# Kernel tuning notes

Hardware: AMD Instinct MI355X
Metric: run time of the kernel (lower is better)

Reference implementation:

```python
import jax, jax.numpy as jnp
import numpy as np

NSTEP = 5

# Clauses (vals = one-hot satisfying truth value per literal):
#   clause 0: ~S(x) | C(x)          vals: L0=[1,0], L1=[0,1]
#   clause 1: ~F(x,y) | ~S(x) | S(y) vals: L0=[1,0], L1=[1,0], L2=[0,1]
# Message to target literal i (torch influence()):
#   msg = w[r] * einsum over shared vars of prod_j ( q[pn_j] . (1 - vals_j) ) outer t_vals

def setup_inputs() -> dict:
    B, N = 2, 2048
    key = jax.random.key(0)
    k1, k2, k3 = jax.random.split(key, 3)
    return {
        "logits_S": jax.random.normal(k1, (B, N, 2), jnp.float32),
        "logits_C": jax.random.normal(k2, (B, N, 2), jnp.float32),
        "logits_F": jax.random.normal(k3, (B, N, N, 2), jnp.float32),
        "weights": jnp.ones((2,), jnp.float32),
    }


def _messages(qS, qC, qF, weights):
    dt = qS.dtype
    e_true = jnp.array([0.0, 1.0], dtype=dt)   # one-hot: positive literal satisfied
    e_false = jnp.array([1.0, 0.0], dtype=dt)  # one-hot: negated literal satisfied
    w0, w1 = weights[0], weights[1]
    # clause 0: ~S(x) | C(x)
    msg_C = (w0 * qS[..., 1])[..., None] * e_true            # [B,N,2]
    msg_S = (w0 * qC[..., 0])[..., None] * e_false           # [B,N,2]
    # clause 1: ~F(x,y) | ~S(x) | S(y)
    # target F(x,y): (q_S[b,x,true]) * (q_S[b,y,false]) on the 'false' slot of F
    msg_F = (w1 * qS[:, :, None, 1] * qS[:, None, :, 0])[..., None] * e_false  # [B,N,N,2]
    # target ~S(x): sum_y q_F[b,x,y,true] * q_S[b,y,false]
    msg_S = msg_S + (w1 * jnp.einsum('bxy,by->bx', qF[..., 1], qS[..., 0]))[..., None] * e_false
    # target S(y): sum_x q_F[b,x,y,true] * q_S[b,x,true]
    msg_S = msg_S + (w1 * jnp.einsum('bxy,bx->by', qF[..., 1], qS[..., 1]))[..., None] * e_true
    return msg_S, msg_C, msg_F


def reference(logits_S, logits_C, logits_F, weights):
    cur_S, cur_C, cur_F = logits_S, logits_C, logits_F
    for _ in range(NSTEP):
        qS = jax.nn.softmax(cur_S, axis=-1)
        qC = jax.nn.softmax(cur_C, axis=-1)
        qF = jax.nn.softmax(cur_F, axis=-1)
        msg_S, msg_C, msg_F = _messages(qS, qC, qF, weights)
        cur_S = logits_S + msg_S
        cur_C = logits_C + msg_C
        cur_F = logits_F + msg_F
    return (cur_S, cur_C, cur_F)
```

## Files before the change

kernel.cpp:

```cpp
#include <hip/hip_runtime.h>

#define NN   2048
#define ROWS 4096
#define RPB  16
#define CSPLIT 4
#define NBY  (ROWS/RPB)
#define PSTR 257
#define NBLK (CSPLIT*NBY)

#define SUBW 32
#define NSUB (NBLK/SUBW)
#define CPAD 16
#define BARSTRIDE ((NSUB+1)*CPAD)
#define NBAR 5
#define SPIN_LIMIT (1<<21)

__device__ __forceinline__ float fsig(float x) {
    float e = __expf(-x);
    return __builtin_amdgcn_rcpf(1.0f + e);
}

__device__ __forceinline__ float gload(const float* p) {
    return __hip_atomic_load(p, __ATOMIC_RELAXED, __HIP_MEMORY_SCOPE_AGENT);
}
__device__ __forceinline__ void gatomic_add(float* p, float v) {
    __hip_atomic_fetch_add(p, v, __ATOMIC_RELAXED, __HIP_MEMORY_SCOPE_AGENT);
}

__device__ __forceinline__ void gridbar(int* cnt, int bid) {
    __syncthreads();
    if (threadIdx.x == 0) {
        asm volatile("" ::: "memory");
        int* sub  = cnt + (bid & (NSUB - 1)) * CPAD;
        int* root = cnt + NSUB * CPAD;
        int old = __hip_atomic_fetch_add(sub, 1, __ATOMIC_RELAXED,
                                         __HIP_MEMORY_SCOPE_AGENT);
        if (old == SUBW - 1)
            __hip_atomic_fetch_add(root, 1, __ATOMIC_RELAXED,
                                   __HIP_MEMORY_SCOPE_AGENT);
        int tries = 0;
        while (__hip_atomic_load(root, __ATOMIC_RELAXED,
                                 __HIP_MEMORY_SCOPE_AGENT) < NSUB) {
            __builtin_amdgcn_s_sleep(1);
            if (++tries > SPIN_LIMIT) break;
        }
        asm volatile("" ::: "memory");
    }
    __syncthreads();
}

template<int T>
__device__ __forceinline__ void do_pass(
    float* __restrict__ stCur, const float* __restrict__ stPrev,
    const float* __restrict__ stPP,
    float* __restrict__ sdif, float* __restrict__ cdif,
    float* __restrict__ part,
    float (&d0)[RPB], float (&d1)[RPB],
    const float4* __restrict__ F,
    const float2* __restrict__ S2, const float2* __restrict__ C2,
    const float* __restrict__ rprev, const float* __restrict__ cprev,
    float* __restrict__ rout, float* __restrict__ cout,
    float4* __restrict__ outF,
    int tid, int sx, int by, int bloc, int row0, int base,
    float w0, float w1)
{
    for (int idx = tid; idx < 512 + RPB; idx += 256) {
        int il = (idx < 512) ? (sx * 512 + idx) : (bloc * RPB + idx - 512);
        int g  = base + il;
        float cur;
        if (T == 0) {
            float2 sv = S2[g], cv = C2[g];
            float sd = sv.y - sv.x;
            sdif[idx] = sd;
            cdif[idx] = cv.x - cv.y;
            cur = fsig(sd);
        } else {
            float rs = gload(rprev + g);
            float cs = gload(cprev + g);
            float qc = (T == 1) ? fsig(cdif[idx])
                                : fsig(cdif[idx] - w0 * stPP[idx]);
            cur = fsig(sdif[idx] + w1*cs - w0*qc - w1*rs);
        }
        stCur[idx] = cur;
    }
    __syncthreads();

    const int j = sx * 256 + tid;
    const float wq0 = 1.0f - stCur[2*tid];
    const float wq1 = 1.0f - stCur[2*tid + 1];
    const float bp0 = (T == 0) ? 0.0f : 1.0f - stPrev[2*tid];
    const float bp1 = (T == 0) ? 0.0f : 1.0f - stPrev[2*tid + 1];

    float c0 = 0.0f, c1 = 0.0f;

#pragma unroll
    for (int i = 0; i < RPB; i++) {
        const float a_c = stCur[512 + i];
        float s0, s1;
        if (T == 0) {
            const float4 f = F[(size_t)(row0 + i) * (NN/2) + j];
            d0[i] = f.y - f.x;
            d1[i] = f.w - f.z;
            s0 = fsig(d0[i]);
            s1 = fsig(d1[i]);
        } else {
            const float m1 = w1 * stPrev[512 + i];
            s0 = fsig(d0[i] - m1 * bp0);
            s1 = fsig(d1[i] - m1 * bp1);
        }
        c0 += s0 * a_c;
        c1 += s1 * a_c;
        part[i * PSTR + tid] = s0 * wq0 + s1 * wq1;
        if (T == 4) {
            const float4 f = F[(size_t)(row0 + i) * (NN/2) + j];
            const float mw = w1 * a_c;
            float4 o;
            o.x = f.x + mw * wq0; o.y = f.y;
            o.z = f.z + mw * wq1; o.w = f.w;
            outF[(size_t)(row0 + i) * (NN/2) + j] = o;
        }
    }

    gatomic_add(cout + base + 2*j,     c0);
    gatomic_add(cout + base + 2*j + 1, c1);

    __syncthreads();
    {
        const int row = tid >> 4, seg = tid & 15;
        float s = 0.0f;
#pragma unroll
        for (int u = 0; u < 16; u++) s += part[row * PSTR + seg * 16 + u];
#pragma unroll
        for (int off = 8; off > 0; off >>= 1) s += __shfl_down(s, off, 16);
        if (seg == 0) gatomic_add(rout + row0 + row, s);
    }
}

__global__ __launch_bounds__(256, 4) void kfused(
    const float4* __restrict__ F,
    const float2* __restrict__ S2, const float2* __restrict__ C2,
    const float* __restrict__ w,
    float* __restrict__ ws,
    float2* __restrict__ outS, float2* __restrict__ outC,
    float4* __restrict__ outF)
{
    __shared__ float st[3][512 + RPB];
    __shared__ float sdif[512 + RPB];
    __shared__ float cdif[512 + RPB];
    __shared__ float part[16 * PSTR];

    const int tid  = threadIdx.x;
    const int sx   = blockIdx.x;
    const int by   = blockIdx.y;
    const int row0 = by * RPB;
    const int b    = by >> 7;
    const int bloc = by & 127;
    const int base = b * NN;
    const int bid  = by * CSPLIT + sx;
    const float w0 = w[0], w1 = w[1];

    float d0[RPB], d1[RPB];

    float* rb = ws;
    float* cb = ws + 5 * ROWS;
    int*   bar = (int*)(ws + 10 * ROWS);
#define RB(t) (rb + (t) * ROWS)
#define CB(t) (cb + (t) * ROWS)

    do_pass<0>(st[0], st[2], st[1], sdif, cdif, part, d0, d1, F, S2, C2,
               nullptr, nullptr, RB(0), CB(0), nullptr,
               tid, sx, by, bloc, row0, base, w0, w1);
    gridbar(bar + 0*BARSTRIDE, bid);
    do_pass<1>(st[1], st[0], st[2], sdif, cdif, part, d0, d1, F, S2, C2,
               RB(0), CB(0), RB(1), CB(1), nullptr,
               tid, sx, by, bloc, row0, base, w0, w1);
    gridbar(bar + 1*BARSTRIDE, bid);
    do_pass<2>(st[2], st[1], st[0], sdif, cdif, part, d0, d1, F, S2, C2,
               RB(1), CB(1), RB(2), CB(2), nullptr,
               tid, sx, by, bloc, row0, base, w0, w1);
    gridbar(bar + 2*BARSTRIDE, bid);
    do_pass<3>(st[0], st[2], st[1], sdif, cdif, part, d0, d1, F, S2, C2,
               RB(2), CB(2), RB(3), CB(3), nullptr,
               tid, sx, by, bloc, row0, base, w0, w1);
    gridbar(bar + 3*BARSTRIDE, bid);
    do_pass<4>(st[1], st[0], st[2], sdif, cdif, part, d0, d1, F, S2, C2,
               RB(3), CB(3), RB(4), CB(4), outF,
               tid, sx, by, bloc, row0, base, w0, w1);
    gridbar(bar + 4*BARSTRIDE, bid);

    if (tid < 4) {
        const int lr = 4 * sx + tid;
        const int g  = row0 + lr;
        const float a4 = st[1][512 + lr];
        const float a3 = st[0][512 + lr];
        const float rs = gload(RB(4) + g);
        const float cs = gload(CB(4) + g);
        const float2 sv = S2[g], cv = C2[g];
        const float qc4 = fsig((cv.x - cv.y) - w0 * a3);
        float2 os, oc;
        os.x = sv.x + w0 * qc4 + w1 * rs;
        os.y = sv.y + w1 * cs;
        oc.x = cv.x;
        oc.y = cv.y + w0 * a4;
        outS[g] = os;
        outC[g] = oc;
    }
}

extern "C" void kernel_launch(void* const* d_in, const int* in_sizes, int n_in,
                              void* d_out, int out_size, void* d_ws, size_t ws_size,
                              hipStream_t stream)
{
    const float2* S2 = (const float2*)d_in[0];
    const float2* C2 = (const float2*)d_in[1];
    const float4* F4 = (const float4*)d_in[2];
    const float*  w  = (const float*)d_in[3];
    float* out = (float*)d_out;
    float* ws  = (float*)d_ws;

    float2* outS = (float2*)out;
    float2* outC = (float2*)(out + 2 * ROWS);
    float4* outF = (float4*)(out + 4 * ROWS);

    hipMemsetAsync(ws, 0,
                   10 * (size_t)ROWS * sizeof(float)
                   + (size_t)NBAR * BARSTRIDE * sizeof(int), stream);

    dim3 gb(CSPLIT, NBY), bb(256, 1, 1);
    void* args[] = { (void*)&F4, (void*)&S2, (void*)&C2, (void*)&w,
                     (void*)&ws, (void*)&outS, (void*)&outC, (void*)&outF };
    hipError_t ce = hipLaunchCooperativeKernel((const void*)kfused, gb, bb,
                                               args, 0, stream);
    if (ce != hipSuccess) {
        (void)hipGetLastError();
        kfused<<<gb, bb, 0, stream>>>(F4, S2, C2, w, ws, outS, outC, outF);
    }
}
```

Before: 208.0 us.

## Split column-sum atomics into four slices, use nontemporal F stores, rotate LDS reads

Column-sum atomic adds are spread across four separate accumulation buffers selected by block row, and readers sum the four slices. This cuts contention among the 128 blocks per batch that all atomically add to the same column addresses each pass. The final F output write now uses nontemporal stores to avoid polluting cache, and the partial-row reduction reads LDS with a rotated index to reduce bank conflicts. The cost is a larger workspace memset and four loads instead of one when consuming column sums.

After: 196.0 us. -5.8%, faster.

```diff
diff --git a/kernel.cpp b/kernel.cpp
--- a/kernel.cpp
+++ b/kernel.cpp
@@ -5,6 +5,7 @@
 #define RPB  16
 #define CSPLIT 4
 #define NBY  (ROWS/RPB)
+#define NCSL 4
 #define PSTR 257
 #define NBLK (CSPLIT*NBY)
 
@@ -14,6 +15,8 @@
 #define BARSTRIDE ((NSUB+1)*CPAD)
 #define NBAR 5
 #define SPIN_LIMIT (1<<21)
+
+typedef float vfloat4 __attribute__((ext_vector_type(4)));
 
 __device__ __forceinline__ float fsig(float x) {
     float e = __expf(-x);
@@ -76,7 +79,9 @@
             cur = fsig(sd);
         } else {
             float rs = gload(rprev + g);
-            float cs = gload(cprev + g);
+            float cs = 0.0f;
+#pragma unroll
+            for (int s = 0; s < NCSL; s++) cs += gload(cprev + s*ROWS + g);
             float qc = (T == 1) ? fsig(cdif[idx])
                                 : fsig(cdif[idx] - w0 * stPP[idx]);
             cur = fsig(sdif[idx] + w1*cs - w0*qc - w1*rs);
@@ -114,22 +119,24 @@
         if (T == 4) {
             const float4 f = F[(size_t)(row0 + i) * (NN/2) + j];
             const float mw = w1 * a_c;
-            float4 o;
+            vfloat4 o;
             o.x = f.x + mw * wq0; o.y = f.y;
             o.z = f.z + mw * wq1; o.w = f.w;
-            outF[(size_t)(row0 + i) * (NN/2) + j] = o;
-        }
-    }
-
-    gatomic_add(cout + base + 2*j,     c0);
-    gatomic_add(cout + base + 2*j + 1, c1);
+            __builtin_nontemporal_store(
+                o, (vfloat4*)&outF[(size_t)(row0 + i) * (NN/2) + j]);
+        }
+    }
+
+    gatomic_add(cout + (by & (NCSL-1))*ROWS + base + 2*j,     c0);
+    gatomic_add(cout + (by & (NCSL-1))*ROWS + base + 2*j + 1, c1);
 
     __syncthreads();
     {
         const int row = tid >> 4, seg = tid & 15;
         float s = 0.0f;
 #pragma unroll
-        for (int u = 0; u < 16; u++) s += part[row * PSTR + seg * 16 + u];
+        for (int u = 0; u < 16; u++)
+            s += part[row * PSTR + seg * 16 + ((seg + u) & 15)];
 #pragma unroll
         for (int off = 8; off > 0; off >>= 1) s += __shfl_down(s, off, 16);
         if (seg == 0) gatomic_add(rout + row0 + row, s);
@@ -163,9 +170,9 @@
 
     float* rb = ws;
     float* cb = ws + 5 * ROWS;
-    int*   bar = (int*)(ws + 10 * ROWS);
+    int*   bar = (int*)(ws + (5 + 5*NCSL) * ROWS);
 #define RB(t) (rb + (t) * ROWS)
-#define CB(t) (cb + (t) * ROWS)
+#define CB(t) (cb + (t) * (NCSL * ROWS))
 
     do_pass<0>(st[0], st[2], st[1], sdif, cdif, part, d0, d1, F, S2, C2,
                nullptr, nullptr, RB(0), CB(0), nullptr,
@@ -194,7 +201,9 @@
         const float a4 = st[1][512 + lr];
         const float a3 = st[0][512 + lr];
         const float rs = gload(RB(4) + g);
-        const float cs = gload(CB(4) + g);
+        float cs = 0.0f;
+#pragma unroll
+        for (int s = 0; s < NCSL; s++) cs += gload(CB(4) + s*ROWS + g);
         const float2 sv = S2[g], cv = C2[g];
         const float qc4 = fsig((cv.x - cv.y) - w0 * a3);
         float2 os, oc;
@@ -222,9 +231,9 @@
     float2* outC = (float2*)(out + 2 * ROWS);
     float4* outF = (float4*)(out + 4 * ROWS);
 
-    hipMemsetAsync(ws, 0,
-                   10 * (size_t)ROWS * sizeof(float)
-                   + (size_t)NBAR * BARSTRIDE * sizeof(int), stream);
+    (void)hipMemsetAsync(ws, 0,
+                         (5 + 5*NCSL) * (size_t)ROWS * sizeof(float)
+                         + (size_t)NBAR * BARSTRIDE * sizeof(int), stream);
 
     dim3 gb(CSPLIT, NBY), bb(256, 1, 1);
     void* args[] = { (void*)&F4, (void*)&S2, (void*)&C2, (void*)&w,
```
